# Kernel tuning notes

Measured on AMD Instinct MI355X. Metric: run time of the kernel, lower is better.

## Reference

```python
import jax, jax.numpy as jnp
import numpy as np

B, H, E, A = 8192, 1024, 300, 512
G = 4  # gates: i, f, o, g


def setup_inputs() -> dict:
    key = jax.random.key(0)
    ks = jax.random.split(key, 9)
    s = lambda fan_in: 1.0 / np.sqrt(fan_in)
    return {
        "h_prev": jax.random.normal(ks[0], (B, H), jnp.float32),
        "c_prev": jax.random.normal(ks[1], (B, H), jnp.float32),
        "embedding_prev": jax.random.normal(ks[2], (B, E), jnp.float32),
        "context": jax.random.normal(ks[3], (B, A), jnp.float32),
        # stacked per-gate weights, torch Linear convention (out, in)
        "Wh": jax.random.normal(ks[4], (G, H, H), jnp.float32) * s(H),
        "Wx": jax.random.normal(ks[5], (G, H, E), jnp.float32) * s(E),
        "Wa": jax.random.normal(ks[6], (G, H, A), jnp.float32) * s(A),
        "bl": jax.random.normal(ks[7], (G, H), jnp.float32) * s(H),  # Linear biases (sum of 3 per gate folded into one is NOT done; see note below)
        "bl2": jax.random.normal(ks[8], (G, H), jnp.float32) * s(E),  # U_* biases
        "bl3": jnp.zeros((G, H), jnp.float32),  # A_* biases (init small) + b_* params (zeros) folded separately
        "bp": jnp.zeros((G, H), jnp.float32),   # the explicit nn.Parameter b_i/b_f/b_o/b_g (init zeros)
    }


def reference(h_prev, c_prev, embedding_prev, context, Wh, Wx, Wa, bl, bl2, bl3, bp):
    # pre[g] = h @ Wh[g].T + x @ Wx[g].T + a @ Wa[g].T + (bl+bl2+bl3+bp)[g]
    pre = (
        jnp.einsum("bi,goi->bgo", h_prev, Wh)
        + jnp.einsum("bi,goi->bgo", embedding_prev, Wx)
        + jnp.einsum("bi,goi->bgo", context, Wa)
        + (bl + bl2 + bl3 + bp)[None]
    )  # [B, 4, H]
    i_t = jax.nn.sigmoid(pre[:, 0])
    f_t = jax.nn.sigmoid(pre[:, 1])
    o_t = jax.nn.sigmoid(pre[:, 2])
    g_t = jnp.tanh(pre[:, 3])
    c_t = f_t * c_prev + i_t * g_t
    h_t = o_t * jnp.tanh(c_t)
    return (h_t, c_t)
```

## Files before the change

### kernel.cpp

```cpp
#include <hip/hip_runtime.h>
#include <stdint.h>

#define B_DIM 8192
#define H_DIM 1024
#define E_DIM 300
#define A_DIM 512
#define KP    1856
#define KE0   1024
#define KA0   1344
#define BM    128
#define BK    64
#define NT    29

typedef __bf16 bf16;
typedef bf16  bf16x8 __attribute__((ext_vector_type(8)));
typedef float f32x4  __attribute__((ext_vector_type(4)));

__device__ __forceinline__ uint16_t f2bf(float f) {
  uint32_t u = __float_as_uint(f);
  u += 0x7fff + ((u >> 16) & 1);
  return (uint16_t)(u >> 16);
}

__global__ void pack_x_kernel(const float* __restrict__ h,
                              const float* __restrict__ e,
                              const float* __restrict__ a,
                              uint16_t* __restrict__ X) {
  int idx = blockIdx.x * blockDim.x + threadIdx.x;
  const int gpr = KP / 8;
  if (idx >= B_DIM * gpr) return;
  int row  = idx / gpr;
  int col0 = (idx % gpr) * 8;
  __align__(16) uint16_t v[8];
#pragma unroll
  for (int j = 0; j < 8; ++j) {
    int c = col0 + j;
    float x;
    if (c < KE0) x = h[(size_t)row * H_DIM + c];
    else if (c < KA0) {
      int ce = c - KE0;
      x = (ce < E_DIM) ? e[(size_t)row * E_DIM + ce] : 0.f;
    } else x = a[(size_t)row * A_DIM + (c - KA0)];
    v[j] = f2bf(x);
  }
  *(uint4*)(X + (size_t)row * KP + col0) = *(const uint4*)v;
}

__global__ void pack_w_kernel(const float* __restrict__ Wh,
                              const float* __restrict__ Wx,
                              const float* __restrict__ Wa,
                              uint16_t* __restrict__ W) {
  int idx = blockIdx.x * blockDim.x + threadIdx.x;
  const int gpr = KP / 8;
  if (idx >= 4096 * gpr) return;
  int row  = idx / gpr;
  int col0 = (idx % gpr) * 8;
  __align__(16) uint16_t v[8];
#pragma unroll
  for (int j = 0; j < 8; ++j) {
    int c = col0 + j;
    float x;
    if (c < KE0) x = Wh[(size_t)row * 1024 + c];
    else if (c < KA0) {
      int ce = c - KE0;
      x = (ce < E_DIM) ? Wx[(size_t)row * E_DIM + ce] : 0.f;
    } else x = Wa[(size_t)row * A_DIM + (c - KA0)];
    v[j] = f2bf(x);
  }
  *(uint4*)(W + (size_t)row * KP + col0) = *(const uint4*)v;
}

__device__ __forceinline__ void async_copy16(const void* g, void* l) {
  __builtin_amdgcn_global_load_lds(
      (__attribute__((address_space(1))) void*)g,
      (__attribute__((address_space(3))) void*)l, 16, 0, 0);
}

__global__ __launch_bounds__(256, 4) void lstm_fused_kernel(
    const uint16_t* __restrict__ X, const uint16_t* __restrict__ W,
    const float* __restrict__ c_prev,
    const float* __restrict__ b0, const float* __restrict__ b1,
    const float* __restrict__ b2, const float* __restrict__ b3,
    float* __restrict__ out) {
  __shared__ __align__(16) uint16_t smem[2 * BM * BK];
  uint16_t* As = smem;
  uint16_t* Bs = smem + BM * BK;
  float*    pre = (float*)smem;

  const int t    = threadIdx.x;
  const int lane = t & 63;
  const int wid  = t >> 6;
  const int wr   = wid >> 1, wc = wid & 1;
  const int m0   = blockIdx.x * BM;
  const int u0   = blockIdx.y * 32;
  const int lr   = lane & 15;
  const int kh   = lane >> 4;

  f32x4 acc[4][4];
#pragma unroll
  for (int n = 0; n < 4; ++n) {
    int cl   = wc * 64 + n * 16 + lr;
    int bidx = (cl >> 5) * H_DIM + u0 + (cl & 31);
    float bs = b0[bidx] + b1[bidx] + b2[bidx] + b3[bidx];
#pragma unroll
    for (int m = 0; m < 4; ++m) acc[m][n] = (f32x4){bs, bs, bs, bs};
  }

  const int sr   = t >> 3;
  const int c8d  = (t & 7) * 8;
  const int csrc = ((t & 7) ^ (sr & 7)) * 8;

  for (int kt = 0; kt < NT; ++kt) {
    const int k0 = kt * BK;
#pragma unroll
    for (int q = 0; q < 4; ++q) {
      async_copy16(X + (size_t)(m0 + q * 32 + sr) * KP + k0 + csrc,
                   As + (q * 32 + sr) * BK + c8d);
      async_copy16(W + (size_t)(q * 1024 + u0 + sr) * KP + k0 + csrc,
                   Bs + (q * 32 + sr) * BK + c8d);
    }
    asm volatile("s_waitcnt vmcnt(0)" ::: "memory");
    __syncthreads();
#pragma unroll
    for (int kk = 0; kk < 2; ++kk) {
      bf16x8 af[4], bfr[4];
#pragma unroll
      for (int m = 0; m < 4; ++m) {
        int row = wr * 64 + m * 16 + lr;
        af[m] = *(const bf16x8*)(As + row * BK + (((kk * 4 + kh) ^ (row & 7)) * 8));
      }
#pragma unroll
      for (int n = 0; n < 4; ++n) {
        int row = wc * 64 + n * 16 + lr;
        bfr[n] = *(const bf16x8*)(Bs + row * BK + (((kk * 4 + kh) ^ (row & 7)) * 8));
      }
#pragma unroll
      for (int m = 0; m < 4; ++m)
#pragma unroll
        for (int n = 0; n < 4; ++n)
          acc[m][n] = __builtin_amdgcn_mfma_f32_16x16x32_bf16(af[m], bfr[n], acc[m][n], 0, 0, 0);
    }
    __syncthreads();
  }

  float* outh = out;
  float* outc = out + (size_t)B_DIM * H_DIM;
  const int eu = t & 31;
  const int rb = (t >> 5) * 8;
#pragma unroll 1
  for (int phase = 0; phase < 2; ++phase) {
    if (wr == phase) {
#pragma unroll
      for (int m = 0; m < 4; ++m)
#pragma unroll
        for (int n = 0; n < 4; ++n) {
          int col = wc * 64 + n * 16 + lr;
#pragma unroll
          for (int j = 0; j < 4; ++j)
            pre[(m * 16 + kh * 4 + j) * 128 + col] = acc[m][n][j];
        }
    }
    __syncthreads();
#pragma unroll 1
    for (int q = 0; q < 8; ++q) {
      int r = rb + q;
      float pi = pre[r * 128 +      eu];
      float pf = pre[r * 128 + 32 + eu];
      float po = pre[r * 128 + 64 + eu];
      float pg = pre[r * 128 + 96 + eu];
      size_t o = (size_t)(m0 + phase * 64 + r) * H_DIM + u0 + eu;
      float cp = c_prev[o];
      float iv = 1.f / (1.f + __expf(-pi));
      float fv = 1.f / (1.f + __expf(-pf));
      float ov = 1.f / (1.f + __expf(-po));
      float gv = tanhf(pg);
      float ct = fv * cp + iv * gv;
      float ht = ov * tanhf(ct);
      outh[o] = ht;
      outc[o] = ct;
    }
    __syncthreads();
  }
}

extern "C" void kernel_launch(void* const* d_in, const int* in_sizes, int n_in,
                              void* d_out, int out_size, void* d_ws, size_t ws_size,
                              hipStream_t stream) {
  const float* h_prev = (const float*)d_in[0];
  const float* c_prev = (const float*)d_in[1];
  const float* emb    = (const float*)d_in[2];
  const float* ctx    = (const float*)d_in[3];
  const float* Wh     = (const float*)d_in[4];
  const float* Wx     = (const float*)d_in[5];
  const float* Wa     = (const float*)d_in[6];
  const float* bl     = (const float*)d_in[7];
  const float* bl2    = (const float*)d_in[8];
  const float* bl3    = (const float*)d_in[9];
  const float* bp     = (const float*)d_in[10];

  uint16_t* X = (uint16_t*)d_ws;
  uint16_t* W = (uint16_t*)((char*)d_ws + (size_t)B_DIM * KP * 2);
  float* out = (float*)d_out;

  {
    int total = B_DIM * (KP / 8);
    pack_x_kernel<<<(total + 255) / 256, 256, 0, stream>>>(h_prev, emb, ctx, X);
  }
  {
    int total = 4096 * (KP / 8);
    pack_w_kernel<<<(total + 255) / 256, 256, 0, stream>>>(Wh, Wx, Wa, W);
  }
  dim3 grid(B_DIM / BM, H_DIM / 32);
  lstm_fused_kernel<<<grid, 256, 0, stream>>>(X, W, c_prev, bl, bl2, bl3, bp, out);
}
```

Before: 178.4 us.

## Enlarge GEMM tile to 256x256 with double-buffered async LDS pipeline

```diff
diff --git a/kernel.cpp b/kernel.cpp
--- a/kernel.cpp
+++ b/kernel.cpp
@@ -5,12 +5,13 @@
 #define H_DIM 1024
 #define E_DIM 300
 #define A_DIM 512
-#define KP    1856
+#define KP    1920
 #define KE0   1024
 #define KA0   1344
-#define BM    128
+#define KA1   1856
 #define BK    64
-#define NT    29
+#define NT    30
+#define NITER 15
 
 typedef __bf16 bf16;
 typedef bf16  bf16x8 __attribute__((ext_vector_type(8)));
@@ -40,7 +41,8 @@
     else if (c < KA0) {
       int ce = c - KE0;
       x = (ce < E_DIM) ? e[(size_t)row * E_DIM + ce] : 0.f;
-    } else x = a[(size_t)row * A_DIM + (c - KA0)];
+    } else if (c < KA1) x = a[(size_t)row * A_DIM + (c - KA0)];
+    else x = 0.f;
     v[j] = f2bf(x);
   }
   *(uint4*)(X + (size_t)row * KP + col0) = *(const uint4*)v;
@@ -53,21 +55,24 @@
   int idx = blockIdx.x * blockDim.x + threadIdx.x;
   const int gpr = KP / 8;
   if (idx >= 4096 * gpr) return;
-  int row  = idx / gpr;
+  int pr   = idx / gpr;
   int col0 = (idx % gpr) * 8;
+  int ub = pr >> 8, g = (pr >> 6) & 3, ui = pr & 63;
+  size_t srow = (size_t)(g * H_DIM + ub * 64 + ui);
   __align__(16) uint16_t v[8];
 #pragma unroll
   for (int j = 0; j < 8; ++j) {
     int c = col0 + j;
     float x;
-    if (c < KE0) x = Wh[(size_t)row * 1024 + c];
+    if (c < KE0) x = Wh[srow * H_DIM + c];
     else if (c < KA0) {
       int ce = c - KE0;
-      x = (ce < E_DIM) ? Wx[(size_t)row * E_DIM + ce] : 0.f;
-    } else x = Wa[(size_t)row * A_DIM + (c - KA0)];
+      x = (ce < E_DIM) ? Wx[srow * E_DIM + ce] : 0.f;
+    } else if (c < KA1) x = Wa[srow * A_DIM + (c - KA0)];
+    else x = 0.f;
     v[j] = f2bf(x);
   }
-  *(uint4*)(W + (size_t)row * KP + col0) = *(const uint4*)v;
+  *(uint4*)(W + (size_t)pr * KP + col0) = *(const uint4*)v;
 }
 
 __device__ __forceinline__ void async_copy16(const void* g, void* l) {
@@ -76,99 +81,144 @@
       (__attribute__((address_space(3))) void*)l, 16, 0, 0);
 }
 
-__global__ __launch_bounds__(256, 4) void lstm_fused_kernel(
+#define WAITV4 asm volatile("s_waitcnt vmcnt(4)" ::: "memory")
+#define WAITV0 asm volatile("s_waitcnt vmcnt(0)" ::: "memory")
+
+#define PHASE(BUF, MP, PRE, TW)                                                              \
+  {                                                                                          \
+    bf16x8 a00 = *(const bf16x8*)(Ard0 + (BUF)*16384 + (2*(MP))*1024);                       \
+    bf16x8 a01 = *(const bf16x8*)(Ard1 + (BUF)*16384 + (2*(MP))*1024);                       \
+    bf16x8 a10 = *(const bf16x8*)(Ard0 + (BUF)*16384 + (2*(MP)+1)*1024);                     \
+    bf16x8 a11 = *(const bf16x8*)(Ard1 + (BUF)*16384 + (2*(MP)+1)*1024);                     \
+    if ((MP) == 0) {                                                                         \
+      _Pragma("unroll")                                                                      \
+      for (int n_ = 0; n_ < 4; ++n_) {                                                       \
+        bfr[n_][0] = *(const bf16x8*)(Brd0 + (BUF)*16384 + n_*1024);                         \
+        bfr[n_][1] = *(const bf16x8*)(Brd1 + (BUF)*16384 + n_*1024);                         \
+      }                                                                                      \
+    }                                                                                        \
+    PRE;                                                                                     \
+    __builtin_amdgcn_s_barrier();                                                            \
+    asm volatile("s_waitcnt lgkmcnt(0)" ::: "memory");                                       \
+    __builtin_amdgcn_s_setprio(1);                                                           \
+    _Pragma("unroll")                                                                        \
+    for (int n_ = 0; n_ < 4; ++n_) {                                                         \
+      acc[2*(MP)][n_]   = __builtin_amdgcn_mfma_f32_16x16x32_bf16(a00, bfr[n_][0], acc[2*(MP)][n_],   0, 0, 0); \
+      acc[2*(MP)+1][n_] = __builtin_amdgcn_mfma_f32_16x16x32_bf16(a10, bfr[n_][0], acc[2*(MP)+1][n_], 0, 0, 0); \
+      acc[2*(MP)][n_]   = __builtin_amdgcn_mfma_f32_16x16x32_bf16(a01, bfr[n_][1], acc[2*(MP)][n_],   0, 0, 0); \
+      acc[2*(MP)+1][n_] = __builtin_amdgcn_mfma_f32_16x16x32_bf16(a11, bfr[n_][1], acc[2*(MP)+1][n_], 0, 0, 0); \
+    }                                                                                        \
+    __builtin_amdgcn_s_setprio(0);                                                           \
+    TW;                                                                                      \
+    __builtin_amdgcn_s_barrier();                                                            \
+  }
+
+__global__ __launch_bounds__(512, 2) void lstm_fused_kernel(
     const uint16_t* __restrict__ X, const uint16_t* __restrict__ W,
     const float* __restrict__ c_prev,
     const float* __restrict__ b0, const float* __restrict__ b1,
     const float* __restrict__ b2, const float* __restrict__ b3,
     float* __restrict__ out) {
-  __shared__ __align__(16) uint16_t smem[2 * BM * BK];
+  __shared__ __align__(16) uint16_t smem[4 * 256 * 64];
   uint16_t* As = smem;
-  uint16_t* Bs = smem + BM * BK;
-  float*    pre = (float*)smem;
+  uint16_t* Bs = smem + 2 * 256 * 64;
 
   const int t    = threadIdx.x;
   const int lane = t & 63;
   const int wid  = t >> 6;
-  const int wr   = wid >> 1, wc = wid & 1;
-  const int m0   = blockIdx.x * BM;
-  const int u0   = blockIdx.y * 32;
+  const int wr   = wid >> 2;
+  const int wc   = wid & 3;
   const int lr   = lane & 15;
   const int kh   = lane >> 4;
-
-  f32x4 acc[4][4];
+  const int m0   = blockIdx.x * 256;
+  const int by   = blockIdx.y;
+  const int n0   = by * 256;
+
+  f32x4 acc[8][4];
 #pragma unroll
   for (int n = 0; n < 4; ++n) {
-    int cl   = wc * 64 + n * 16 + lr;
-    int bidx = (cl >> 5) * H_DIM + u0 + (cl & 31);
+    int bidx = wc * H_DIM + by * 64 + n * 16 + lr;
     float bs = b0[bidx] + b1[bidx] + b2[bidx] + b3[bidx];
 #pragma unroll
-    for (int m = 0; m < 4; ++m) acc[m][n] = (f32x4){bs, bs, bs, bs};
+    for (int m = 0; m < 8; ++m) acc[m][n] = (f32x4){bs, bs, bs, bs};
   }
 
   const int sr   = t >> 3;
-  const int c8d  = (t & 7) * 8;
-  const int csrc = ((t & 7) ^ (sr & 7)) * 8;
-
-  for (int kt = 0; kt < NT; ++kt) {
-    const int k0 = kt * BK;
-#pragma unroll
-    for (int q = 0; q < 4; ++q) {
-      async_copy16(X + (size_t)(m0 + q * 32 + sr) * KP + k0 + csrc,
-                   As + (q * 32 + sr) * BK + c8d);
-      async_copy16(W + (size_t)(q * 1024 + u0 + sr) * KP + k0 + csrc,
-                   Bs + (q * 32 + sr) * BK + c8d);
-    }
-    asm volatile("s_waitcnt vmcnt(0)" ::: "memory");
-    __syncthreads();
-#pragma unroll
-    for (int kk = 0; kk < 2; ++kk) {
-      bf16x8 af[4], bfr[4];
-#pragma unroll
-      for (int m = 0; m < 4; ++m) {
-        int row = wr * 64 + m * 16 + lr;
-        af[m] = *(const bf16x8*)(As + row * BK + (((kk * 4 + kh) ^ (row & 7)) * 8));
-      }
-#pragma unroll
-      for (int n = 0; n < 4; ++n) {
-        int row = wc * 64 + n * 16 + lr;
-        bfr[n] = *(const bf16x8*)(Bs + row * BK + (((kk * 4 + kh) ^ (row & 7)) * 8));
-      }
-#pragma unroll
-      for (int m = 0; m < 4; ++m)
-#pragma unroll
-        for (int n = 0; n < 4; ++n)
-          acc[m][n] = __builtin_amdgcn_mfma_f32_16x16x32_bf16(af[m], bfr[n], acc[m][n], 0, 0, 0);
-    }
-    __syncthreads();
-  }
-
+  const int csrc = (((t & 7) ^ (sr & 7)) * 8);
+
+  auto stageA = [&](int kt, int hf, int buf) {
+#pragma unroll
+    for (int l_ = 0; l_ < 2; ++l_)
+      async_copy16(X + (size_t)(m0 + hf * 128 + l_ * 64 + sr) * KP + kt * BK + csrc,
+                   As + buf * 16384 + (hf * 128 + l_ * 64) * 64 + t * 8);
+  };
+  auto stageB = [&](int kt, int hf, int buf) {
+#pragma unroll
+    for (int l_ = 0; l_ < 2; ++l_)
+      async_copy16(W + (size_t)(n0 + hf * 128 + l_ * 64 + sr) * KP + kt * BK + csrc,
+                   Bs + buf * 16384 + (hf * 128 + l_ * 64) * 64 + t * 8);
+  };
+
+  const int ck0 = (kh ^ (lr & 7)) * 8;
+  const uint16_t* Ard0 = As + (wr * 128 + lr) * 64 + ck0;
+  const uint16_t* Ard1 = As + (wr * 128 + lr) * 64 + (ck0 ^ 32);
+  const uint16_t* Brd0 = Bs + (wc * 64 + lr) * 64 + ck0;
+  const uint16_t* Brd1 = Bs + (wc * 64 + lr) * 64 + (ck0 ^ 32);
+
+  bf16x8 bfr[4][2];
+
+  stageB(0, 0, 0); stageB(0, 1, 0);
+  stageA(0, 0, 0); stageA(0, 1, 0);
+  stageB(1, 0, 1); stageB(1, 1, 1);
+  WAITV4;
+  __builtin_amdgcn_s_barrier();
+
+#pragma unroll 1
+  for (int it = 0; it < NITER; ++it) {
+    const int kt = 2 * it;
+    const bool ntail = (it < NITER - 1);
+    PHASE(0, 0, stageA(kt + 1, 0, 1), (void)0)
+    PHASE(0, 1, stageA(kt + 1, 1, 1), (void)0)
+    PHASE(0, 2, if (ntail) stageB(kt + 2, 0, 0), (void)0)
+    PHASE(0, 3, if (ntail) stageB(kt + 2, 1, 0),
+          if (ntail) { WAITV4; } else { WAITV0; })
+    PHASE(1, 0, if (ntail) stageA(kt + 2, 0, 0), (void)0)
+    PHASE(1, 1, if (ntail) stageA(kt + 2, 1, 0), (void)0)
+    PHASE(1, 2, if (ntail) stageB(kt + 3, 0, 1), (void)0)
+    PHASE(1, 3, if (ntail) stageB(kt + 3, 1, 1),
+          if (ntail) { WAITV4; })
+  }
+
+  float* pre  = (float*)smem;
   float* outh = out;
   float* outc = out + (size_t)B_DIM * H_DIM;
-  const int eu = t & 31;
-  const int rb = (t >> 5) * 8;
+  const int eu   = lane;
+  const int wrow = wid * 16;
 #pragma unroll 1
-  for (int phase = 0; phase < 2; ++phase) {
-    if (wr == phase) {
-#pragma unroll
-      for (int m = 0; m < 4; ++m)
+  for (int ph = 0; ph < 2; ++ph) {
+    if (wr == ph) {
+#pragma unroll
+      for (int m = 0; m < 8; ++m)
 #pragma unroll
         for (int n = 0; n < 4; ++n) {
-          int col = wc * 64 + n * 16 + lr;
+          int row = m * 16 + kh * 4;
+          int col = (wc * 64 + n * 16 + lr) ^ (kh << 4);
 #pragma unroll
           for (int j = 0; j < 4; ++j)
-            pre[(m * 16 + kh * 4 + j) * 128 + col] = acc[m][n][j];
+            pre[(row + j) * 256 + col] = acc[m][n][j];
         }
     }
     __syncthreads();
 #pragma unroll 1
-    for (int q = 0; q < 8; ++q) {
-      int r = rb + q;
-      float pi = pre[r * 128 +      eu];
-      float pf = pre[r * 128 + 32 + eu];
-      float po = pre[r * 128 + 64 + eu];
-      float pg = pre[r * 128 + 96 + eu];
-      size_t o = (size_t)(m0 + phase * 64 + r) * H_DIM + u0 + eu;
+    for (int q = 0; q < 16; ++q) {
+      int r   = wrow + q;
+      int swz = (r & 12) << 2;
+      int ec  = eu ^ swz;
+      float pi = pre[r * 256 + ec];
+      float pf = pre[r * 256 + 64 + ec];
+      float po = pre[r * 256 + 128 + ec];
+      float pg = pre[r * 256 + 192 + ec];
+      size_t o = (size_t)(m0 + ph * 128 + r) * H_DIM + by * 64 + eu;
       float cp = c_prev[o];
       float iv = 1.f / (1.f + __expf(-pi));
       float fv = 1.f / (1.f + __expf(-pf));
@@ -210,6 +260,6 @@
     int total = 4096 * (KP / 8);
     pack_w_kernel<<<(total + 255) / 256, 256, 0, stream>>>(Wh, Wx, Wa, W);
   }
-  dim3 grid(B_DIM / BM, H_DIM / 32);
-  lstm_fused_kernel<<<grid, 256, 0, stream>>>(X, W, c_prev, bl, bl2, bl3, bp, out);
-}
+  dim3 grid(B_DIM / 256, 4096 / 256);
+  lstm_fused_kernel<<<grid, 512, 0, stream>>>(X, W, c_prev, bl, bl2, bl3, bp, out);
+}
```

Measured after the change: 183.5 us. 2.9% more time.
